# Performance work log

Measured on AMD Instinct MI355X. Metric: run time of the kernel, lower is better.

Reference implementation:

```python
import jax, jax.numpy as jnp
import numpy as np

T, B, DIM, N = 2048, 16, 1024, 64


def setup_inputs() -> dict:
    key = jax.random.key(0)
    ks = jax.random.split(key, 6)
    # xavier-uniform-ish scale for [N, DIM] linear weights
    lim = float(np.sqrt(6.0 / (DIM + N)))
    mk = lambda k: jax.random.uniform(k, (N, DIM), jnp.float32, -lim, lim)
    return {
        "x": jax.random.normal(ks[0], (T, B, DIM), jnp.float32),
        "S": jnp.zeros((B, N, N), jnp.float32),
        "W_k": mk(ks[1]),
        "W_v": mk(ks[2]),
        "W_q": mk(ks[3]),
        "W_alpha": mk(ks[4]),
        "d_alpha": jnp.full((N,), 0.1, jnp.float32),
        "b_alpha": jnp.full((N,), 2.0, jnp.float32),
    }


def reference(x, S, W_k, W_v, W_q, W_alpha, d_alpha, b_alpha):
    # Projections for the whole sequence at once: [T, B, N]
    k_all = jnp.einsum('tbd,nd->tbn', x, W_k)
    v_all = jnp.einsum('tbd,nd->tbn', x, W_v)
    q_all = jnp.einsum('tbd,nd->tbn', x, W_q)
    a_all = jnp.einsum('tbd,nd->tbn', x, W_alpha)

    def step(S, inp):
        k, v, q, ax = inp  # each [B, N]
        retrieved = jnp.einsum('bij,bj->bi', S, k)                 # [B, N]
        alpha = jax.nn.sigmoid(ax + d_alpha * retrieved + b_alpha)  # [B, N]
        outer_vk = v[:, :, None] * k[:, None, :]                    # [B, N, N]
        S = alpha[:, :, None] * S + (1.0 - alpha[:, :, None]) * outer_vk
        out = jnp.einsum('bij,bj->bi', S, q)                        # [B, N]
        out = out * jax.nn.silu(out)
        return S, out

    S_final, output = jax.lax.scan(step, S, (k_all, v_all, q_all, a_all))
    return output, S_final
```

## Files before the change

### kernel.cpp

```cpp
#include <hip/hip_runtime.h>
#include <hip/hip_bf16.h>

#define T_STEPS 2048
#define BATCH 16
#define DIM 1024
#define NDIM 64
#define M_TOTAL (T_STEPS * BATCH)
#define STRIDE (BATCH * NDIM)
#define CH 32

typedef __attribute__((ext_vector_type(8))) short bf16x8;
typedef __attribute__((ext_vector_type(4))) float f32x4;
typedef __attribute__((ext_vector_type(2))) float f32x2;

__device__ inline unsigned pk_bf(float lo, float hi) {
    __hip_bfloat162 h = __float22bfloat162_rn(float2{lo, hi});
    return *(unsigned*)&h;
}

template <int CTRL>
__device__ inline float dpp_add(float x) {
    int v = __builtin_amdgcn_update_dpp(0, __float_as_int(x), CTRL, 0xF, 0xF, true);
    return x + __int_as_float(v);
}
__device__ inline float red16(float x) {
    x = dpp_add<0xB1>(x);
    x = dpp_add<0x4E>(x);
    x = dpp_add<0x141>(x);
    x = dpp_add<0x140>(x);
    return x;
}
__device__ inline float fast_sigmoid(float z) {
    return __builtin_amdgcn_rcpf(1.f + __expf(-z));
}

#define AS1 __attribute__((address_space(1)))
#define AS3 __attribute__((address_space(3)))
__device__ inline void gl_lds16(const float* g, float* l) {
    __builtin_amdgcn_global_load_lds((const AS1 unsigned*)g, (AS3 unsigned*)l, 16, 0, 0);
}
__device__ inline void gl_lds16s(const unsigned short* g, unsigned short* l) {
    __builtin_amdgcn_global_load_lds((const AS1 unsigned*)g, (AS3 unsigned*)l, 16, 0, 0);
}
__device__ inline void gl_lds4(const float* g, float* l) {
    __builtin_amdgcn_global_load_lds((const AS1 unsigned*)g, (AS3 unsigned*)l, 4, 0, 0);
}
#define WAIT_VM0 do { __builtin_amdgcn_s_waitcnt(0x0F70); asm volatile("" ::: "memory"); } while (0)

__global__ __launch_bounds__(256) void pack_w(
    const float* __restrict__ Wk, const float* __restrict__ Wq,
    const float* __restrict__ Wv, const float* __restrict__ Wa,
    unsigned short* __restrict__ Wb) {
    int n = blockIdx.x;
    int sel = n >> 6;
    const float* W = (sel == 0) ? Wk : (sel == 1) ? Wq : (sel == 2) ? Wv : Wa;
    int k4 = threadIdx.x * 4;
    float4 f = *(const float4*)(W + (size_t)(n & 63) * DIM + k4);
    uint2 u;
    u.x = pk_bf(f.x, f.y);
    u.y = pk_bf(f.z, f.w);
    *(uint2*)(Wb + (size_t)n * DIM + k4) = u;
}

__global__ __launch_bounds__(256, 2) void proj_kernel(
    const float* __restrict__ x, const unsigned short* __restrict__ Wb,
    const float* __restrict__ ba, float* __restrict__ Kp, float* __restrict__ Qp,
    float* __restrict__ VAi) {
    __shared__ float sA[128 * 64];
    __shared__ unsigned short sB[128 * 64];

    const int m0 = blockIdx.x * 128;
    const int ntile = blockIdx.y;
    const int tid = threadIdx.x;
    const int wv = tid >> 6, lane = tid & 63, lrow = lane & 15, quad = lane >> 4;
    const int wm = wv & 1, wn = wv >> 1;

    f32x4 acc[4][4];
#pragma unroll
    for (int a = 0; a < 4; a++)
#pragma unroll
        for (int b = 0; b < 4; b++) acc[a][b] = (f32x4)(0.f);

    const float* xg = x + (size_t)(m0 + (tid >> 4)) * DIM + (tid & 15) * 4;
    const unsigned short* wg = Wb + (size_t)(ntile * 128 + (tid >> 3)) * DIM + (tid & 7) * 8;

    for (int it = 0; it < 16; ++it) {
        const int k0 = it * 64;
        __syncthreads();
#pragma unroll
        for (int j = 0; j < 8; ++j)
            gl_lds16(xg + (size_t)(16 * j) * DIM + k0, &sA[(tid + 256 * j) * 4]);
#pragma unroll
        for (int j = 0; j < 4; ++j)
            gl_lds16s(wg + (size_t)(32 * j) * DIM + k0, &sB[(tid + 256 * j) * 8]);
        WAIT_VM0;
        __syncthreads();

#pragma unroll
        for (int ks = 0; ks < 2; ++ks) {
            bf16x8 af[4];
#pragma unroll
            for (int mt = 0; mt < 4; ++mt) {
                const float* pa = &sA[(wm * 64 + mt * 16 + lrow) * 64 + ks * 32 + quad * 8];
                float4 lo = ((const float4*)pa)[0], hi = ((const float4*)pa)[1];
                unsigned pk[4] = {pk_bf(lo.x, lo.y), pk_bf(lo.z, lo.w),
                                  pk_bf(hi.x, hi.y), pk_bf(hi.z, hi.w)};
                af[mt] = *(bf16x8*)pk;
            }
#pragma unroll
            for (int nt = 0; nt < 4; ++nt) {
                bf16x8 bfr = *(const bf16x8*)&sB[(wn * 64 + nt * 16 + lrow) * 64 + ks * 32 + quad * 8];
#pragma unroll
                for (int mt = 0; mt < 4; ++mt)
                    acc[mt][nt] = __builtin_amdgcn_mfma_f32_16x16x32_bf16(af[mt], bfr, acc[mt][nt], 0, 0, 0);
            }
        }
    }

    const int g2 = ntile * 2 + wn;
    float bav[4];
    if (g2 == 3) {
#pragma unroll
        for (int nt = 0; nt < 4; ++nt) bav[nt] = ba[nt * 16 + lrow];
    }
#pragma unroll
    for (int mt = 0; mt < 4; ++mt)
#pragma unroll
        for (int nt = 0; nt < 4; ++nt) {
            int col = nt * 16 + lrow;
#pragma unroll
            for (int reg = 0; reg < 4; ++reg) {
                int m = m0 + wm * 64 + mt * 16 + quad * 4 + reg;
                float vvv = acc[mt][nt][reg];
                if (g2 == 0) Kp[(size_t)m * 64 + col] = vvv;
                else if (g2 == 1) Qp[(size_t)m * 64 + col] = vvv;
                else if (g2 == 2) VAi[(size_t)m * 128 + col * 2] = vvv;
                else VAi[(size_t)m * 128 + col * 2 + 1] = vvv + bav[nt];
            }
        }
}

__global__ __launch_bounds__(256) void kq_kernel(
    const float* __restrict__ Kp, const float* __restrict__ Qp, float* __restrict__ kq) {
    int m = blockIdx.x * 16 + (threadIdx.x >> 4);
    int c = threadIdx.x & 15;
    float4 k = *(const float4*)(Kp + (size_t)m * 64 + c * 4);
    float4 q = *(const float4*)(Qp + (size_t)m * 64 + c * 4);
    float p = k.x * q.x + k.y * q.y + k.z * q.z + k.w * q.w;
    p = red16(p);
    if (c == 0) kq[m] = p;
}

__global__ __launch_bounds__(64, 1) void recur_kernel(
    const float* __restrict__ Kp, const float* __restrict__ Qp,
    const float* __restrict__ VAi, const float* __restrict__ KQp,
    const float* __restrict__ S0, const float* __restrict__ d_alpha,
    float* __restrict__ out, float* __restrict__ Sout) {
    __shared__ float Kl[2][CH][64];
    __shared__ float Ql[2][CH][64];
    __shared__ float VAl[2][CH][8];
    __shared__ float KQl[2][64];
    __shared__ float Ol[CH][4];

    int b = blockIdx.y, g = blockIdx.x, lane = threadIdx.x;
    int r = lane >> 4, c = lane & 15, i = g * 4 + r, c4 = c * 4;

    float4 sv = *(const float4*)(S0 + ((size_t)b * NDIM + i) * NDIM + c4);
    f32x2 s01 = {sv.x, sv.y}, s23 = {sv.z, sv.w};
    float da = d_alpha[i];

    const float* Kbase = Kp + (size_t)b * NDIM + (size_t)(lane >> 4) * STRIDE + (lane & 15) * 4;
    const float* Qbase = Qp + (size_t)b * NDIM + (size_t)(lane >> 4) * STRIDE + (lane & 15) * 4;
    const float* VAbase = VAi + (size_t)b * 128 + g * 8 + (lane & 1) * 4 + (size_t)(lane >> 1) * 2048;
    const float* KQbase = KQp + b + (size_t)(lane & 31) * BATCH;

    auto load_chunk = [&](int t0, int buf) {
#pragma unroll
        for (int j = 0; j < 8; ++j) {
            gl_lds16(Kbase + (size_t)(t0 + j * 4) * STRIDE, &Kl[buf][j * 4][0]);
            gl_lds16(Qbase + (size_t)(t0 + j * 4) * STRIDE, &Ql[buf][j * 4][0]);
        }
        gl_lds16(VAbase + (size_t)t0 * 2048, &VAl[buf][0][0]);
        gl_lds4(KQbase + (size_t)t0 * BATCH, &KQl[buf][0]);
    };

    load_chunk(0, 0);
    WAIT_VM0;

    f32x2 k01[2], k23[2], q01[2], q23[2], va[2];
    float kqv[2];
    {
        const float* Kb = &Kl[0][0][0];
        const float* Qb = &Ql[0][0][0];
#pragma unroll
        for (int u = 0; u < 2; ++u) {
            f32x4 kk = *(const f32x4*)(Kb + u * 64 + c4);
            f32x4 qq = *(const f32x4*)(Qb + u * 64 + c4);
            k01[u] = kk.lo; k23[u] = kk.hi;
            q01[u] = qq.lo; q23[u] = qq.hi;
            va[u] = *(const f32x2*)&VAl[0][u][r * 2];
            kqv[u] = KQl[0][u];
        }
    }

    for (int j = 0; j < T_STEPS / CH; ++j) {
        int cb = j & 1;
        if (j + 1 < T_STEPS / CH) load_chunk((j + 1) * CH, cb ^ 1);

        const float* Kb = &Kl[cb][0][0];
        const float* Qb = &Ql[cb][0][0];
        const float* Vb = &VAl[cb][0][0];
        const float* Qk = &KQl[cb][0];

#pragma unroll
        for (int tl = 0; tl < CH; ++tl) {
            int sl = tl & 1;
            f32x2 k0v = k01[sl], k1v = k23[sl], q0v = q01[sl], q1v = q23[sl];
            f32x2 vva = va[sl];
            float kq = kqv[sl];
            if (tl < CH - 2) {
                f32x4 kk = *(const f32x4*)(Kb + (tl + 2) * 64 + c4);
                f32x4 qq = *(const f32x4*)(Qb + (tl + 2) * 64 + c4);
                k01[sl] = kk.lo; k23[sl] = kk.hi;
                q01[sl] = qq.lo; q23[sl] = qq.hi;
                va[sl] = *(const f32x2*)&Vb[(tl + 2) * 8 + r * 2];
                kqv[sl] = Qk[tl + 2];
            }

            f32x2 pk_ = k0v * s01;
            pk_ = k1v * s23 + pk_;
            f32x2 pq_ = q0v * s01;
            pq_ = q1v * s23 + pq_;
            float rk = red16(pk_.x + pk_.y);
            float rq = red16(pq_.x + pq_.y);

            float v = vva.x;
            f32x2 w01 = v * k0v, w23 = v * k1v;
            f32x2 d01 = s01 - w01, d23 = s23 - w23;

            float alpha = fast_sigmoid(fmaf(da, rk, vva.y));
            f32x2 a2 = {alpha, alpha};
            s01 = w01 + a2 * d01;
            s23 = w23 + a2 * d23;

            float u1 = (1.f - alpha) * v;
            float o = fmaf(alpha, rq, u1 * kq);
            float ov = o * o * fast_sigmoid(o);
            if (c == 0) Ol[tl][r] = ov;
        }
        WAIT_VM0;

        if (lane < 32) {
            float4 t4 = *(const float4*)&Ol[lane][0];
            *(float4*)(out + ((size_t)(j * CH + lane) * BATCH + b) * NDIM + g * 4) = t4;
        }

        if (j + 1 < T_STEPS / CH) {
            int nb = cb ^ 1;
            const float* Kn = &Kl[nb][0][0];
            const float* Qn = &Ql[nb][0][0];
#pragma unroll
            for (int u = 0; u < 2; ++u) {
                f32x4 kk = *(const f32x4*)(Kn + u * 64 + c4);
                f32x4 qq = *(const f32x4*)(Qn + u * 64 + c4);
                k01[u] = kk.lo; k23[u] = kk.hi;
                q01[u] = qq.lo; q23[u] = qq.hi;
                va[u] = *(const f32x2*)&VAl[nb][u][r * 2];
                kqv[u] = KQl[nb][u];
            }
        }
    }

    float* so = Sout + ((size_t)b * NDIM + i) * NDIM + c4;
    *(float4*)so = float4{s01.x, s01.y, s23.x, s23.y};
}

extern "C" void kernel_launch(void* const* d_in, const int* in_sizes, int n_in,
                              void* d_out, int out_size, void* d_ws, size_t ws_size,
                              hipStream_t stream) {
    const float* x  = (const float*)d_in[0];
    const float* S0 = (const float*)d_in[1];
    const float* Wk = (const float*)d_in[2];
    const float* Wv = (const float*)d_in[3];
    const float* Wq = (const float*)d_in[4];
    const float* Wa = (const float*)d_in[5];
    const float* da = (const float*)d_in[6];
    const float* ba = (const float*)d_in[7];

    float* out = (float*)d_out;
    float* Sout = out + (size_t)T_STEPS * BATCH * NDIM;

    const size_t per = (size_t)M_TOTAL * NDIM;
    float* Kp  = (float*)d_ws;
    float* Qp  = Kp + per;
    float* VAi = Qp + per;
    float* kq  = VAi + 2 * per;
    unsigned short* Wb = (unsigned short*)(kq + M_TOTAL);

    pack_w<<<dim3(256), dim3(256), 0, stream>>>(Wk, Wq, Wv, Wa, Wb);
    proj_kernel<<<dim3(M_TOTAL / 128, 2), dim3(256), 0, stream>>>(x, Wb, ba, Kp, Qp, VAi);
    kq_kernel<<<dim3(M_TOTAL / 16), dim3(256), 0, stream>>>(Kp, Qp, kq);
    recur_kernel<<<dim3(16, BATCH), dim3(64), 0, stream>>>(Kp, Qp, VAi, kq, S0, da, out, Sout);
}
```

Measured before the change: 493.9 us.

## Restructure projection GEMM tiling, convert x once, double chunk size and fold log2e

```diff
diff --git a/kernel.cpp b/kernel.cpp
--- a/kernel.cpp
+++ b/kernel.cpp
@@ -7,7 +7,8 @@
 #define NDIM 64
 #define M_TOTAL (T_STEPS * BATCH)
 #define STRIDE (BATCH * NDIM)
-#define CH 32
+#define CH 64
+#define NLOG2E -1.44269504088896340736f
 
 typedef __attribute__((ext_vector_type(8))) short bf16x8;
 typedef __attribute__((ext_vector_type(4))) float f32x4;
@@ -30,16 +31,10 @@
     x = dpp_add<0x140>(x);
     return x;
 }
-__device__ inline float fast_sigmoid(float z) {
-    return __builtin_amdgcn_rcpf(1.f + __expf(-z));
-}
 
 #define AS1 __attribute__((address_space(1)))
 #define AS3 __attribute__((address_space(3)))
 __device__ inline void gl_lds16(const float* g, float* l) {
-    __builtin_amdgcn_global_load_lds((const AS1 unsigned*)g, (AS3 unsigned*)l, 16, 0, 0);
-}
-__device__ inline void gl_lds16s(const unsigned short* g, unsigned short* l) {
     __builtin_amdgcn_global_load_lds((const AS1 unsigned*)g, (AS3 unsigned*)l, 16, 0, 0);
 }
 __device__ inline void gl_lds4(const float* g, float* l) {
@@ -62,18 +57,17 @@
     *(uint2*)(Wb + (size_t)n * DIM + k4) = u;
 }
 
+#define LDA 40
 __global__ __launch_bounds__(256, 2) void proj_kernel(
     const float* __restrict__ x, const unsigned short* __restrict__ Wb,
     const float* __restrict__ ba, float* __restrict__ Kp, float* __restrict__ Qp,
     float* __restrict__ VAi) {
-    __shared__ float sA[128 * 64];
-    __shared__ unsigned short sB[128 * 64];
-
-    const int m0 = blockIdx.x * 128;
-    const int ntile = blockIdx.y;
+    __shared__ unsigned short sA[2][64 * LDA];
+    __shared__ unsigned short sB[2][256 * LDA];
+
+    const int m0 = blockIdx.x * 64;
     const int tid = threadIdx.x;
-    const int wv = tid >> 6, lane = tid & 63, lrow = lane & 15, quad = lane >> 4;
-    const int wm = wv & 1, wn = wv >> 1;
+    const int wn = tid >> 6, lane = tid & 63, lrow = lane & 15, quad = lane >> 4;
 
     f32x4 acc[4][4];
 #pragma unroll
@@ -81,45 +75,58 @@
 #pragma unroll
         for (int b = 0; b < 4; b++) acc[a][b] = (f32x4)(0.f);
 
-    const float* xg = x + (size_t)(m0 + (tid >> 4)) * DIM + (tid & 15) * 4;
-    const unsigned short* wg = Wb + (size_t)(ntile * 128 + (tid >> 3)) * DIM + (tid & 7) * 8;
-
-    for (int it = 0; it < 16; ++it) {
-        const int k0 = it * 64;
+    const int ar = tid >> 2;
+    const int acb = (tid & 3) * 8;
+    const float* xg = x + (size_t)(m0 + ar) * DIM + acb;
+    const unsigned short* wg = Wb + (size_t)tid * DIM;
+
+    float4 a4[2];
+    uint4 b4[4];
+    auto load_globals = [&](int it) {
+        const int k0 = it * 32;
+        a4[0] = *(const float4*)(xg + k0);
+        a4[1] = *(const float4*)(xg + k0 + 4);
+#pragma unroll
+        for (int j = 0; j < 4; ++j) b4[j] = *(const uint4*)(wg + k0 + j * 8);
+    };
+    auto cvt_store = [&](int buf) {
+        unsigned ap[4];
+        ap[0] = pk_bf(a4[0].x, a4[0].y);
+        ap[1] = pk_bf(a4[0].z, a4[0].w);
+        ap[2] = pk_bf(a4[1].x, a4[1].y);
+        ap[3] = pk_bf(a4[1].z, a4[1].w);
+        *(uint4*)&sA[buf][ar * LDA + acb] = *(uint4*)&ap[0];
+#pragma unroll
+        for (int j = 0; j < 4; ++j)
+            *(uint4*)&sB[buf][tid * LDA + j * 8] = b4[j];
+    };
+
+    load_globals(0);
+    cvt_store(0);
+    __syncthreads();
+
+    for (int it = 0; it < 32; ++it) {
+        const int cur = it & 1;
+        if (it < 31) load_globals(it + 1);
+
+        bf16x8 af[4];
+#pragma unroll
+        for (int mt = 0; mt < 4; ++mt)
+            af[mt] = *(const bf16x8*)&sA[cur][(mt * 16 + lrow) * LDA + quad * 8];
+#pragma unroll
+        for (int nt = 0; nt < 4; ++nt) {
+            bf16x8 bfr = *(const bf16x8*)&sB[cur][(wn * 64 + nt * 16 + lrow) * LDA + quad * 8];
+#pragma unroll
+            for (int mt = 0; mt < 4; ++mt)
+                acc[mt][nt] = __builtin_amdgcn_mfma_f32_16x16x32_bf16(af[mt], bfr, acc[mt][nt], 0, 0, 0);
+        }
+
+        if (it < 31) cvt_store(cur ^ 1);
         __syncthreads();
-#pragma unroll
-        for (int j = 0; j < 8; ++j)
-            gl_lds16(xg + (size_t)(16 * j) * DIM + k0, &sA[(tid + 256 * j) * 4]);
-#pragma unroll
-        for (int j = 0; j < 4; ++j)
-            gl_lds16s(wg + (size_t)(32 * j) * DIM + k0, &sB[(tid + 256 * j) * 8]);
-        WAIT_VM0;
-        __syncthreads();
-
-#pragma unroll
-        for (int ks = 0; ks < 2; ++ks) {
-            bf16x8 af[4];
-#pragma unroll
-            for (int mt = 0; mt < 4; ++mt) {
-                const float* pa = &sA[(wm * 64 + mt * 16 + lrow) * 64 + ks * 32 + quad * 8];
-                float4 lo = ((const float4*)pa)[0], hi = ((const float4*)pa)[1];
-                unsigned pk[4] = {pk_bf(lo.x, lo.y), pk_bf(lo.z, lo.w),
-                                  pk_bf(hi.x, hi.y), pk_bf(hi.z, hi.w)};
-                af[mt] = *(bf16x8*)pk;
-            }
-#pragma unroll
-            for (int nt = 0; nt < 4; ++nt) {
-                bf16x8 bfr = *(const bf16x8*)&sB[(wn * 64 + nt * 16 + lrow) * 64 + ks * 32 + quad * 8];
-#pragma unroll
-                for (int mt = 0; mt < 4; ++mt)
-                    acc[mt][nt] = __builtin_amdgcn_mfma_f32_16x16x32_bf16(af[mt], bfr, acc[mt][nt], 0, 0, 0);
-            }
-        }
     }
 
-    const int g2 = ntile * 2 + wn;
     float bav[4];
-    if (g2 == 3) {
+    if (wn == 3) {
 #pragma unroll
         for (int nt = 0; nt < 4; ++nt) bav[nt] = ba[nt * 16 + lrow];
     }
@@ -130,12 +137,12 @@
             int col = nt * 16 + lrow;
 #pragma unroll
             for (int reg = 0; reg < 4; ++reg) {
-                int m = m0 + wm * 64 + mt * 16 + quad * 4 + reg;
+                int m = m0 + mt * 16 + quad * 4 + reg;
                 float vvv = acc[mt][nt][reg];
-                if (g2 == 0) Kp[(size_t)m * 64 + col] = vvv;
-                else if (g2 == 1) Qp[(size_t)m * 64 + col] = vvv;
-                else if (g2 == 2) VAi[(size_t)m * 128 + col * 2] = vvv;
-                else VAi[(size_t)m * 128 + col * 2 + 1] = vvv + bav[nt];
+                if (wn == 0) Kp[(size_t)m * 64 + col] = vvv;
+                else if (wn == 1) Qp[(size_t)m * 64 + col] = vvv;
+                else if (wn == 2) VAi[(size_t)m * 128 + col * 2] = vvv;
+                else VAi[(size_t)m * 128 + col * 2 + 1] = NLOG2E * (vvv + bav[nt]);
             }
         }
 }
@@ -159,7 +166,7 @@
     __shared__ float Kl[2][CH][64];
     __shared__ float Ql[2][CH][64];
     __shared__ float VAl[2][CH][8];
-    __shared__ float KQl[2][64];
+    __shared__ float KQl[2][CH];
     __shared__ float Ol[CH][4];
 
     int b = blockIdx.y, g = blockIdx.x, lane = threadIdx.x;
@@ -167,20 +174,21 @@
 
     float4 sv = *(const float4*)(S0 + ((size_t)b * NDIM + i) * NDIM + c4);
     f32x2 s01 = {sv.x, sv.y}, s23 = {sv.z, sv.w};
-    float da = d_alpha[i];
+    float dabar = d_alpha[i] * NLOG2E;
 
     const float* Kbase = Kp + (size_t)b * NDIM + (size_t)(lane >> 4) * STRIDE + (lane & 15) * 4;
     const float* Qbase = Qp + (size_t)b * NDIM + (size_t)(lane >> 4) * STRIDE + (lane & 15) * 4;
     const float* VAbase = VAi + (size_t)b * 128 + g * 8 + (lane & 1) * 4 + (size_t)(lane >> 1) * 2048;
-    const float* KQbase = KQp + b + (size_t)(lane & 31) * BATCH;
+    const float* KQbase = KQp + b + (size_t)lane * BATCH;
 
     auto load_chunk = [&](int t0, int buf) {
 #pragma unroll
-        for (int j = 0; j < 8; ++j) {
+        for (int j = 0; j < 16; ++j) {
             gl_lds16(Kbase + (size_t)(t0 + j * 4) * STRIDE, &Kl[buf][j * 4][0]);
             gl_lds16(Qbase + (size_t)(t0 + j * 4) * STRIDE, &Ql[buf][j * 4][0]);
         }
         gl_lds16(VAbase + (size_t)t0 * 2048, &VAl[buf][0][0]);
+        gl_lds16(VAbase + (size_t)(t0 + 32) * 2048, &VAl[buf][32][0]);
         gl_lds4(KQbase + (size_t)t0 * BATCH, &KQl[buf][0]);
     };
 
@@ -189,18 +197,14 @@
 
     f32x2 k01[2], k23[2], q01[2], q23[2], va[2];
     float kqv[2];
-    {
-        const float* Kb = &Kl[0][0][0];
-        const float* Qb = &Ql[0][0][0];
-#pragma unroll
-        for (int u = 0; u < 2; ++u) {
-            f32x4 kk = *(const f32x4*)(Kb + u * 64 + c4);
-            f32x4 qq = *(const f32x4*)(Qb + u * 64 + c4);
-            k01[u] = kk.lo; k23[u] = kk.hi;
-            q01[u] = qq.lo; q23[u] = qq.hi;
-            va[u] = *(const f32x2*)&VAl[0][u][r * 2];
-            kqv[u] = KQl[0][u];
-        }
+#pragma unroll
+    for (int u = 0; u < 2; ++u) {
+        f32x4 kk = *(const f32x4*)(&Kl[0][u][c4]);
+        f32x4 qq = *(const f32x4*)(&Ql[0][u][c4]);
+        k01[u] = kk.lo; k23[u] = kk.hi;
+        q01[u] = qq.lo; q23[u] = qq.hi;
+        va[u] = *(const f32x2*)&VAl[0][u][r * 2];
+        kqv[u] = KQl[0][u];
     }
 
     for (int j = 0; j < T_STEPS / CH; ++j) {
@@ -228,41 +232,43 @@
             }
 
             f32x2 pk_ = k0v * s01;
+            f32x2 pq_ = q0v * s01;
             pk_ = k1v * s23 + pk_;
-            f32x2 pq_ = q0v * s01;
             pq_ = q1v * s23 + pq_;
-            float rk = red16(pk_.x + pk_.y);
-            float rq = red16(pq_.x + pq_.y);
+            float rk = pk_.x + pk_.y;
+            float rq = pq_.x + pq_.y;
+            rk = dpp_add<0xB1>(rk);  rq = dpp_add<0xB1>(rq);
+            rk = dpp_add<0x4E>(rk);  rq = dpp_add<0x4E>(rq);
+            rk = dpp_add<0x141>(rk); rq = dpp_add<0x141>(rq);
+            rk = dpp_add<0x140>(rk); rq = dpp_add<0x140>(rq);
 
             float v = vva.x;
             f32x2 w01 = v * k0v, w23 = v * k1v;
             f32x2 d01 = s01 - w01, d23 = s23 - w23;
 
-            float alpha = fast_sigmoid(fmaf(da, rk, vva.y));
+            float e = __builtin_amdgcn_exp2f(fmaf(dabar, rk, vva.y));
+            float alpha = __builtin_amdgcn_rcpf(1.f + e);
             f32x2 a2 = {alpha, alpha};
-            s01 = w01 + a2 * d01;
-            s23 = w23 + a2 * d23;
-
-            float u1 = (1.f - alpha) * v;
+            s01 = a2 * d01 + w01;
+            s23 = a2 * d23 + w23;
+
+            float u1 = fmaf(-alpha, v, v);
             float o = fmaf(alpha, rq, u1 * kq);
-            float ov = o * o * fast_sigmoid(o);
+            float so = __builtin_amdgcn_rcpf(1.f + __builtin_amdgcn_exp2f(o * NLOG2E));
+            float ov = o * o * so;
             if (c == 0) Ol[tl][r] = ov;
         }
         WAIT_VM0;
 
-        if (lane < 32) {
-            float4 t4 = *(const float4*)&Ol[lane][0];
-            *(float4*)(out + ((size_t)(j * CH + lane) * BATCH + b) * NDIM + g * 4) = t4;
-        }
+        float4 t4 = *(const float4*)&Ol[lane][0];
+        *(float4*)(out + ((size_t)(j * CH + lane) * BATCH + b) * NDIM + g * 4) = t4;
 
         if (j + 1 < T_STEPS / CH) {
             int nb = cb ^ 1;
-            const float* Kn = &Kl[nb][0][0];
-            const float* Qn = &Ql[nb][0][0];
 #pragma unroll
             for (int u = 0; u < 2; ++u) {
-                f32x4 kk = *(const f32x4*)(Kn + u * 64 + c4);
-                f32x4 qq = *(const f32x4*)(Qn + u * 64 + c4);
+                f32x4 kk = *(const f32x4*)(&Kl[nb][u][c4]);
+                f32x4 qq = *(const f32x4*)(&Ql[nb][u][c4]);
                 k01[u] = kk.lo; k23[u] = kk.hi;
                 q01[u] = qq.lo; q23[u] = qq.hi;
                 va[u] = *(const f32x2*)&VAl[nb][u][r * 2];
@@ -298,7 +304,7 @@
     unsigned short* Wb = (unsigned short*)(kq + M_TOTAL);
 
     pack_w<<<dim3(256), dim3(256), 0, stream>>>(Wk, Wq, Wv, Wa, Wb);
-    proj_kernel<<<dim3(M_TOTAL / 128, 2), dim3(256), 0, stream>>>(x, Wb, ba, Kp, Qp, VAi);
+    proj_kernel<<<dim3(M_TOTAL / 64), dim3(256), 0, stream>>>(x, Wb, ba, Kp, Qp, VAi);
     kq_kernel<<<dim3(M_TOTAL / 16), dim3(256), 0, stream>>>(Kp, Qp, kq);
     recur_kernel<<<dim3(16, BATCH), dim3(64), 0, stream>>>(Kp, Qp, VAi, kq, S0, da, out, Sout);
 }
```

Measured after the change: 556.4 us. 12.6% more time.
